# Optimization experiments

Measured on AMD Instinct MI355X. Metric: run time of the kernel, lower is better.

The kernel has to match this reference:

```python
import jax, jax.numpy as jnp
import numpy as np

TAU = 2.0          # LIF membrane time constant (spikingjelly default)
ALPHA = 2.0        # ATan surrogate width
EPS = 1e-5         # BatchNorm eps
NUM_HEADS = 8
SCALE = 0.125

@jax.custom_vjp
def spike(x):
    return (x >= 0.0).astype(x.dtype)

def _spike_fwd(x):
    return (x >= 0.0).astype(x.dtype), x

def _spike_bwd(x, g):
    # ATan surrogate gradient (spikingjelly default)
    return (g * (ALPHA / 2.0) / (1.0 + (jnp.pi / 2.0 * ALPHA * x) ** 2),)

spike.defvjp(_spike_fwd, _spike_bwd)

def lif(x, v_th):
    # Multi-step LIF over leading time axis T; hard reset to 0, v_reset=0.
    def step(v, xt):
        h = v + (xt - v) / TAU
        s = spike(h - v_th)
        return h * (1.0 - s), s
    _, s = jax.lax.scan(step, jnp.zeros_like(x[0]), x)
    return s

def bn(x, g, b, m, v):
    # BatchNorm1d in eval mode over channel (last) dim
    return (x - m) * jax.lax.rsqrt(v + EPS) * g + b

def setup_inputs() -> dict:
    key = jax.random.key(0)
    ks = jax.random.split(key, 16)
    T, B, N, C = 4, 16, 512, 512
    s = 1.0 / np.sqrt(C)
    inp = {"x": jax.random.normal(ks[0], (T, B, N, C), jnp.float32)}
    for i, p in enumerate("qkvp"):
        inp[f"w{p}"] = jax.random.normal(ks[1 + i], (C, C), jnp.float32) * s
        inp[f"b{p}"] = jnp.zeros((C,), jnp.float32)
        inp[f"{p}_gamma"] = jnp.ones((C,), jnp.float32)
        inp[f"{p}_beta"] = jnp.zeros((C,), jnp.float32)
        inp[f"{p}_mean"] = jax.random.normal(ks[5 + i], (C,), jnp.float32) * 0.1
        inp[f"{p}_var"] = jax.random.uniform(ks[9 + i], (C,), jnp.float32, minval=0.5, maxval=1.5)
    return inp

def reference(x, wq, bq, q_gamma, q_beta, q_mean, q_var,
              wk, bk, k_gamma, k_beta, k_mean, k_var,
              wv, bv, v_gamma, v_beta, v_mean, v_var,
              wp, bp, p_gamma, p_beta, p_mean, p_var):
    T, B, N, C = x.shape
    H = NUM_HEADS
    D = C // H

    def branch(w, b, g, be, m, va):
        y = bn(x @ w.T + b, g, be, m, va)          # Linear -> BN1d (eval)
        y = lif(y, 1.0)                             # spiking activation
        return y.reshape(T, B, N, H, D).transpose(0, 1, 3, 2, 4)  # [T,B,H,N,D]

    q = branch(wq, bq, q_gamma, q_beta, q_mean, q_var)
    k = branch(wk, bk, k_gamma, k_beta, k_mean, k_var)
    v = branch(wv, bv, v_gamma, v_beta, v_mean, v_var)

    attn = jnp.einsum('tbhnd,tbhmd->tbhnm', q, k) * SCALE  # [T,B,H,N,N]
    o = jnp.einsum('tbhnm,tbhmd->tbhnd', attn, v)          # [T,B,H,N,D]
    o = o.transpose(0, 1, 3, 2, 4).reshape(T, B, N, C)
    o = lif(o, 0.5)                                        # attn_lif, v_th=0.5
    o = bn(o @ wp.T + bp, p_gamma, p_beta, p_mean, p_var)
    return lif(o, 1.0)
```

## Files before the change

### kernel.cpp

```cpp
#include <hip/hip_runtime.h>
#include <hip/hip_bf16.h>
#include <hip/hip_fp16.h>
#include <cstddef>
#include <cstdint>

#define T_ 4
#define B_ 16
#define N_ 512
#define C_ 512
#define H_ 8
#define D_ 64
#define BN_T (B_*N_)

typedef unsigned short u16;
typedef __attribute__((ext_vector_type(8))) short bf16x8;
typedef __attribute__((ext_vector_type(8))) _Float16 f16x8;
typedef __attribute__((ext_vector_type(8))) unsigned short u16x8;
typedef __attribute__((ext_vector_type(4))) float f32x4;

__device__ __forceinline__ u16 f2bf_exact(float f) {
    union { float f; unsigned u; } x; x.f = f; return (u16)(x.u >> 16);
}
__device__ __forceinline__ void split2(float f, u16& h1, u16& h2) {
    const __half a = __float2half(f);
    const float r = (f - __half2float(a)) * 2048.0f;
    const __half b = __float2half(r);
    h1 = __half_as_ushort(a); h2 = __half_as_ushort(b);
}
__device__ __forceinline__ int swz(int rr, int q) {
    return (rr << 6) + (((q ^ ((rr >> 1) & 3)) & 3) << 4);
}
__device__ __forceinline__ int SW(int row, int col) {
    return (row << 6) + (col ^ ((row & 7) << 3));
}
__device__ __forceinline__ void gload16(const void* g, void* l) {
    __builtin_amdgcn_global_load_lds(
        (const __attribute__((address_space(1))) unsigned int*)g,
        (__attribute__((address_space(3))) unsigned int*)l, 16, 0, 0);
}

__global__ __launch_bounds__(256) void k_split_x(
    const float* __restrict__ x, u16* __restrict__ x1t, u16* __restrict__ x2t)
{
    const int tile = blockIdx.x;
    const int mt = tile >> 4, kb = tile & 15;
    const int tid = threadIdx.x;
    const int rr = tid >> 1, kh = tid & 1;
    const int t = rr & 3, bn = mt * 32 + (rr >> 2);
    const float* src = x + ((size_t)t * BN_T + bn) * C_ + kb * 32 + kh * 16;
    float f[16];
    *reinterpret_cast<float4*>(f + 0)  = *reinterpret_cast<const float4*>(src + 0);
    *reinterpret_cast<float4*>(f + 4)  = *reinterpret_cast<const float4*>(src + 4);
    *reinterpret_cast<float4*>(f + 8)  = *reinterpret_cast<const float4*>(src + 8);
    *reinterpret_cast<float4*>(f + 12) = *reinterpret_cast<const float4*>(src + 12);
    char* d1 = (char*)(x1t + ((size_t)tile << 12));
    char* d2 = (char*)(x2t + ((size_t)tile << 12));
    #pragma unroll
    for (int j = 0; j < 2; ++j) {
        u16x8 p1, p2;
        #pragma unroll
        for (int e = 0; e < 8; ++e) { u16 h1, h2; split2(f[8*j+e], h1, h2); p1[e] = h1; p2[e] = h2; }
        const int q = 2 * kh + j;
        *reinterpret_cast<u16x8*>(d1 + swz(rr, q)) = p1;
        *reinterpret_cast<u16x8*>(d2 + swz(rr, q)) = p2;
    }
}

__global__ __launch_bounds__(256) void k_split_w(
    const float* __restrict__ w, u16* __restrict__ w1t, u16* __restrict__ w2t)
{
    const int tile = blockIdx.x;
    const int nt = tile >> 4, kb = tile & 15;
    const int tid = threadIdx.x;
    const int rr = tid >> 1, kh = tid & 1;
    const int c = nt * 128 + rr;
    const float* src = w + (size_t)c * C_ + kb * 32 + kh * 16;
    float f[16];
    *reinterpret_cast<float4*>(f + 0)  = *reinterpret_cast<const float4*>(src + 0);
    *reinterpret_cast<float4*>(f + 4)  = *reinterpret_cast<const float4*>(src + 4);
    *reinterpret_cast<float4*>(f + 8)  = *reinterpret_cast<const float4*>(src + 8);
    *reinterpret_cast<float4*>(f + 12) = *reinterpret_cast<const float4*>(src + 12);
    char* d1 = (char*)(w1t + ((size_t)tile << 12));
    char* d2 = (char*)(w2t + ((size_t)tile << 12));
    #pragma unroll
    for (int j = 0; j < 2; ++j) {
        u16x8 p1, p2;
        #pragma unroll
        for (int e = 0; e < 8; ++e) { u16 h1, h2; split2(f[8*j+e], h1, h2); p1[e] = h1; p2[e] = h2; }
        const int q = 2 * kh + j;
        *reinterpret_cast<u16x8*>(d1 + swz(rr, q)) = p1;
        *reinterpret_cast<u16x8*>(d2 + swz(rr, q)) = p2;
    }
}

template<int MODE>
__global__ __launch_bounds__(256, 2) void k_linear_mfma(
    const u16* __restrict__ a1t, const u16* __restrict__ a2t,
    const u16* __restrict__ w1t, const u16* __restrict__ w2t,
    const float* __restrict__ bias, const float* __restrict__ gamma,
    const float* __restrict__ beta, const float* __restrict__ mean,
    const float* __restrict__ var, void* __restrict__ outp)
{
    __shared__ u16 lds[2][4][4096];

    const int dd  = blockIdx.x;
    const int lid = (dd & 7) * 128 + (dd >> 3);
    const int mt  = lid >> 2;
    const int nt  = lid & 3;
    const int bn0 = mt * 32;
    const int c0  = nt * 128;

    const int tid = threadIdx.x;
    const int wv  = tid >> 6, lane = tid & 63;
    const int l15 = tid & 15, g = (tid & 63) >> 4;
    const int go  = wv * 2048 + lane * 16;
    const int lo  = wv * 2048;

    f32x4 accA[2][8], accB[2][8];
    #pragma unroll
    for (int rt = 0; rt < 2; ++rt)
        #pragma unroll
        for (int ct = 0; ct < 8; ++ct) { accA[rt][ct] = {0,0,0,0}; accB[rt][ct] = {0,0,0,0}; }

    const size_t abase = (size_t)mt * 16, bbase = (size_t)nt * 16;

    auto stage = [&](int buf, int kb) {
        char* L = (char*)&lds[buf][0][0];
        const char* ga1 = (const char*)(a1t + ((abase + kb) << 12)) + go;
        const char* gb1 = (const char*)(w1t + ((bbase + kb) << 12)) + go;
        const char* gb2 = (const char*)(w2t + ((bbase + kb) << 12)) + go;
        gload16(ga1,        L + lo);
        gload16(ga1 + 1024, L + lo + 1024);
        if (MODE == 0) {
            const char* ga2 = (const char*)(a2t + ((abase + kb) << 12)) + go;
            gload16(ga2,        L + 8192 + lo);
            gload16(ga2 + 1024, L + 8192 + lo + 1024);
        }
        gload16(gb1,        L + 16384 + lo);
        gload16(gb1 + 1024, L + 16384 + lo + 1024);
        gload16(gb2,        L + 24576 + lo);
        gload16(gb2 + 1024, L + 24576 + lo + 1024);
    };

    stage(0, 0);
    __syncthreads();

    #pragma unroll 1
    for (int kb = 0; kb < 16; ++kb) {
        const int buf = kb & 1;
        if (kb < 15) stage(buf ^ 1, kb + 1);
        const char* L = (const char*)&lds[buf][0][0];
        f16x8 a1[2], a2[2];
        #pragma unroll
        for (int rt = 0; rt < 2; ++rt) {
            const int rr = wv * 32 + rt * 16 + l15;
            a1[rt] = *reinterpret_cast<const f16x8*>(L + swz(rr, g));
            if (MODE == 0)
                a2[rt] = *reinterpret_cast<const f16x8*>(L + 8192 + swz(rr, g));
        }
        #pragma unroll
        for (int ct = 0; ct < 8; ++ct) {
            const int rr2 = ct * 16 + l15;
            const f16x8 b1 = *reinterpret_cast<const f16x8*>(L + 16384 + swz(rr2, g));
            const f16x8 b2 = *reinterpret_cast<const f16x8*>(L + 24576 + swz(rr2, g));
            #pragma unroll
            for (int rt = 0; rt < 2; ++rt) {
                accA[rt][ct] = __builtin_amdgcn_mfma_f32_16x16x32_f16(a1[rt], b1, accA[rt][ct], 0, 0, 0);
                if (MODE == 0)
                    accB[rt][ct] = __builtin_amdgcn_mfma_f32_16x16x32_f16(a2[rt], b1, accB[rt][ct], 0, 0, 0);
                accB[rt][ct] = __builtin_amdgcn_mfma_f32_16x16x32_f16(a1[rt], b2, accB[rt][ct], 0, 0, 0);
            }
        }
        __syncthreads();
    }

    #pragma unroll
    for (int ct = 0; ct < 8; ++ct) {
        const int c = c0 + ct * 16 + l15;
        const float rs = 1.0f / sqrtf(var[c] + 1e-5f);
        const float ga = gamma[c], be = beta[c], mu = mean[c], bi = bias[c];
        #pragma unroll
        for (int rt = 0; rt < 2; ++rt) {
            const int bn = bn0 + wv * 8 + rt * 4 + g;
            float vm = 0.f;
            #pragma unroll
            for (int r = 0; r < 4; ++r) {
                const float y = accA[rt][ct][r] + accB[rt][ct][r] * (1.0f / 2048.0f) + bi;
                const float ybn = (y - mu) * rs * ga + be;
                const float h = vm + (ybn - vm) * 0.5f;
                const bool sp = (h >= 1.0f);
                vm = sp ? 0.f : h;
                if (MODE == 0) {
                    const int b = bn >> 9, n = bn & 511;
                    const int hh = c >> 6, d2 = c & 63;
                    ((u16*)outp)[((((size_t)r * B_ + b) * H_ + hh) * N_ + n) * D_ + d2] = sp ? 0x3F80 : 0;
                } else {
                    ((float*)outp)[((size_t)r * BN_T + bn) * C_ + c] = sp ? 1.0f : 0.0f;
                }
            }
        }
    }
}

__global__ __launch_bounds__(256) void k_attn_mfma(
    const u16* __restrict__ qg, const u16* __restrict__ kg,
    const u16* __restrict__ vg, u16* __restrict__ s2t)
{
    __shared__ u16 ks[4096];
    __shared__ u16 vts[4096];
    __shared__ u16 ssb[4096];

    const int id  = blockIdx.x;
    const int lid = (id & 7) * 128 + (id >> 3);
    const int bh  = lid >> 3;
    const int n0  = (lid & 7) * 64;
    const int b   = bh >> 3, hh = bh & 7;

    const int tid  = threadIdx.x;
    const int w    = tid >> 6, lane = tid & 63;
    const int l15  = lane & 15, g = lane >> 4;
    const int krow = tid >> 4, kcol = (tid & 15) * 4;
    const int vkv  = (tid & 15) * 4, vd = (tid >> 4) * 4;

    f32x4 vmem[4], oacc[4];
    #pragma unroll
    for (int d0 = 0; d0 < 4; ++d0) { vmem[d0] = {0,0,0,0}; oacc[d0] = {0,0,0,0}; }

    ushort4 kpre[4], vpre[4];
    bf16x8 qpre[2], qa[2];

    auto prefetch = [&](int it2) {
        const int t2 = it2 >> 3, m0 = (it2 & 7) * 64;
        const size_t base2 = ((size_t)t2 * (B_ * H_) + bh) * (size_t)(N_ * D_);
        #pragma unroll
        for (int i = 0; i < 4; ++i)
            kpre[i] = *reinterpret_cast<const ushort4*>(kg + base2 + (size_t)(m0 + krow + 16 * i) * D_ + kcol);
        #pragma unroll
        for (int i = 0; i < 4; ++i)
            vpre[i] = *reinterpret_cast<const ushort4*>(vg + base2 + (size_t)(m0 + vkv + i) * D_ + vd);
        if ((it2 & 7) == 0) {
            qpre[0] = *reinterpret_cast<const bf16x8*>(qg + base2 + (size_t)(n0 + 16 * w + l15) * D_ + 8 * g);
            qpre[1] = *reinterpret_cast<const bf16x8*>(qg + base2 + (size_t)(n0 + 16 * w + l15) * D_ + 32 + 8 * g);
        }
    };

    prefetch(0);

    #pragma unroll 1
    for (int it = 0; it < 32; ++it) {
        const int t = it >> 3, jt = it & 7;
        if (jt == 0) { qa[0] = qpre[0]; qa[1] = qpre[1]; }

        #pragma unroll
        for (int i = 0; i < 4; ++i) {
            const int row = krow + 16 * i;
            *reinterpret_cast<ushort4*>(&ks[SW(row, kcol)]) = kpre[i];
        }
        #pragma unroll
        for (int j = 0; j < 4; ++j) {
            ushort4 wv4;
            wv4.x = (&vpre[0].x)[j]; wv4.y = (&vpre[1].x)[j];
            wv4.z = (&vpre[2].x)[j]; wv4.w = (&vpre[3].x)[j];
            *reinterpret_cast<ushort4*>(&vts[SW(vd + j, vkv)]) = wv4;
        }
        __syncthreads();
        if (it < 31) prefetch(it + 1);

        #pragma unroll
        for (int kvt = 0; kvt < 4; ++kvt) {
            f32x4 acc = {0.f, 0.f, 0.f, 0.f};
            #pragma unroll
            for (int c = 0; c < 2; ++c) {
                const bf16x8 kb = *reinterpret_cast<const bf16x8*>(
                    &ks[SW(16 * kvt + l15, 32 * c + 8 * g)]);
                acc = __builtin_amdgcn_mfma_f32_16x16x32_bf16(qa[c], kb, acc, 0, 0, 0);
            }
            #pragma unroll
            for (int r = 0; r < 4; ++r)
                ssb[w * 1024 + SW(4 * g + r, 16 * kvt + l15)] = f2bf_exact(acc[r] * 0.125f);
        }
        #pragma unroll
        for (int c = 0; c < 2; ++c) {
            const bf16x8 sa = *reinterpret_cast<const bf16x8*>(
                &ssb[w * 1024 + SW(l15, 32 * c + 8 * g)]);
            #pragma unroll
            for (int d0 = 0; d0 < 4; ++d0) {
                const bf16x8 vb = *reinterpret_cast<const bf16x8*>(
                    &vts[SW(16 * d0 + l15, 32 * c + 8 * g)]);
                oacc[d0] = __builtin_amdgcn_mfma_f32_16x16x32_bf16(sa, vb, oacc[d0], 0, 0, 0);
            }
        }
        __syncthreads();

        if (jt == 7) {
            #pragma unroll
            for (int d0 = 0; d0 < 4; ++d0) {
                const int c = hh * 64 + d0 * 16 + l15;
                const int kb2 = c >> 5, kq = (c >> 3) & 3, e = c & 7;
                #pragma unroll
                for (int r = 0; r < 4; ++r) {
                    const float h = vmem[d0][r] + (oacc[d0][r] - vmem[d0][r]) * 0.5f;
                    const bool sp = (h >= 0.5f);
                    vmem[d0][r] = sp ? 0.f : h;
                    const int n = n0 + 16 * w + 4 * g + r;
                    const int bn = b * 512 + n;
                    const int mt2 = bn >> 5;
                    const int rr2 = (bn & 31) * 4 + t;
                    const size_t off = (((size_t)mt2 * 16 + kb2) << 13) + (rr2 << 6)
                                     + (((kq ^ ((rr2 >> 1) & 3)) & 3) << 4) + (e << 1);
                    *(u16*)((char*)s2t + off) = sp ? 0x3C00 : 0;
                }
                oacc[d0] = {0.f, 0.f, 0.f, 0.f};
            }
        }
    }
}

extern "C" void kernel_launch(void* const* d_in, const int* in_sizes, int n_in,
                              void* d_out, int out_size, void* d_ws, size_t ws_size,
                              hipStream_t stream)
{
    const float* x = (const float*)d_in[0];
    const float* W[4]  = {(const float*)d_in[1],  (const float*)d_in[7],  (const float*)d_in[13], (const float*)d_in[19]};
    const float* Bi[4] = {(const float*)d_in[2],  (const float*)d_in[8],  (const float*)d_in[14], (const float*)d_in[20]};
    const float* Ga[4] = {(const float*)d_in[3],  (const float*)d_in[9],  (const float*)d_in[15], (const float*)d_in[21]};
    const float* Be[4] = {(const float*)d_in[4],  (const float*)d_in[10], (const float*)d_in[16], (const float*)d_in[22]};
    const float* Mu[4] = {(const float*)d_in[5],  (const float*)d_in[11], (const float*)d_in[17], (const float*)d_in[23]};
    const float* Va[4] = {(const float*)d_in[6],  (const float*)d_in[12], (const float*)d_in[18], (const float*)d_in[24]};

    const size_t SPK = (size_t)T_ * B_ * N_ * C_;
    const size_t WSZ = (size_t)C_ * C_;
    u16* qb  = (u16*)d_ws;
    u16* kbf = qb + SPK;
    u16* vbf = kbf + SPK;
    u16* x1t = vbf + SPK;
    u16* x2t = x1t + SPK;
    u16* wt  = x2t + SPK;
    u16* s2t = x1t;

    dim3 blk(256);
    k_split_x<<<4096, blk, 0, stream>>>(x, x1t, x2t);
    for (int i = 0; i < 4; ++i)
        k_split_w<<<64, blk, 0, stream>>>(W[i], wt + (2*i) * WSZ, wt + (2*i+1) * WSZ);

    k_linear_mfma<0><<<1024, blk, 0, stream>>>(x1t, x2t, wt + 0*WSZ, wt + 1*WSZ, Bi[0], Ga[0], Be[0], Mu[0], Va[0], qb);
    k_linear_mfma<0><<<1024, blk, 0, stream>>>(x1t, x2t, wt + 2*WSZ, wt + 3*WSZ, Bi[1], Ga[1], Be[1], Mu[1], Va[1], kbf);
    k_linear_mfma<0><<<1024, blk, 0, stream>>>(x1t, x2t, wt + 4*WSZ, wt + 5*WSZ, Bi[2], Ga[2], Be[2], Mu[2], Va[2], vbf);
    k_attn_mfma<<<1024, blk, 0, stream>>>(qb, kbf, vbf, s2t);
    k_linear_mfma<1><<<1024, blk, 0, stream>>>(s2t, x2t, wt + 6*WSZ, wt + 7*WSZ, Bi[3], Ga[3], Be[3], Mu[3], Va[3], d_out);
}
```

Before: 322.3 us.

## Restructure attention kernel with 512-thread blocks and double-buffered software pipeline

The attention kernel now runs 512 threads per block, each block covering 128 query rows, and launches half as many blocks. Half the threads load K tiles and the other half load V tiles. K, V and score tiles are double-buffered so that the QK^T product for tile j+1 overlaps the PV product for tile j, with one barrier pair per step. The 0.125 scale moves from the bf16 scores to the final accumulator, which changes where bf16 rounding happens. The cost is more LDS per block and fewer blocks, which may lower occupancy.

Result: no change. 323.4 us (+0.3%).

```diff
diff --git a/kernel.cpp b/kernel.cpp
--- a/kernel.cpp
+++ b/kernel.cpp
@@ -202,115 +202,141 @@
     }
 }
 
-__global__ __launch_bounds__(256) void k_attn_mfma(
+__global__ __launch_bounds__(512, 4) void k_attn_mfma(
     const u16* __restrict__ qg, const u16* __restrict__ kg,
     const u16* __restrict__ vg, u16* __restrict__ s2t)
 {
-    __shared__ u16 ks[4096];
-    __shared__ u16 vts[4096];
-    __shared__ u16 ssb[4096];
+    __shared__ u16 ks[2][4096];
+    __shared__ u16 vts[2][4096];
+    __shared__ u16 ssb[8][2][1024];
 
     const int id  = blockIdx.x;
-    const int lid = (id & 7) * 128 + (id >> 3);
-    const int bh  = lid >> 3;
-    const int n0  = (lid & 7) * 64;
+    const int lid = (id & 7) * 64 + (id >> 3);
+    const int bh  = lid >> 2;
+    const int qt  = lid & 3;
     const int b   = bh >> 3, hh = bh & 7;
 
     const int tid  = threadIdx.x;
     const int w    = tid >> 6, lane = tid & 63;
     const int l15  = lane & 15, g = lane >> 4;
-    const int krow = tid >> 4, kcol = (tid & 15) * 4;
-    const int vkv  = (tid & 15) * 4, vd = (tid >> 4) * 4;
+
+    const bool isK = (tid < 256);
+    const int st   = isK ? tid : tid - 256;
+    const int krow = st >> 4, kcol = (st & 15) * 4;
+    const int vkv  = (st & 15) * 4, vd = (st >> 4) * 4;
+
+    ushort4 pre[4];
+    bf16x8 qa[2];
 
     f32x4 vmem[4], oacc[4];
     #pragma unroll
-    for (int d0 = 0; d0 < 4; ++d0) { vmem[d0] = {0,0,0,0}; oacc[d0] = {0,0,0,0}; }
-
-    ushort4 kpre[4], vpre[4];
-    bf16x8 qpre[2], qa[2];
-
-    auto prefetch = [&](int it2) {
-        const int t2 = it2 >> 3, m0 = (it2 & 7) * 64;
-        const size_t base2 = ((size_t)t2 * (B_ * H_) + bh) * (size_t)(N_ * D_);
-        #pragma unroll
-        for (int i = 0; i < 4; ++i)
-            kpre[i] = *reinterpret_cast<const ushort4*>(kg + base2 + (size_t)(m0 + krow + 16 * i) * D_ + kcol);
-        #pragma unroll
-        for (int i = 0; i < 4; ++i)
-            vpre[i] = *reinterpret_cast<const ushort4*>(vg + base2 + (size_t)(m0 + vkv + i) * D_ + vd);
-        if ((it2 & 7) == 0) {
-            qpre[0] = *reinterpret_cast<const bf16x8*>(qg + base2 + (size_t)(n0 + 16 * w + l15) * D_ + 8 * g);
-            qpre[1] = *reinterpret_cast<const bf16x8*>(qg + base2 + (size_t)(n0 + 16 * w + l15) * D_ + 32 + 8 * g);
-        }
-    };
-
-    prefetch(0);
+    for (int d0 = 0; d0 < 4; ++d0) vmem[d0] = {0,0,0,0};
 
     #pragma unroll 1
-    for (int it = 0; it < 32; ++it) {
-        const int t = it >> 3, jt = it & 7;
-        if (jt == 0) { qa[0] = qpre[0]; qa[1] = qpre[1]; }
-
-        #pragma unroll
-        for (int i = 0; i < 4; ++i) {
-            const int row = krow + 16 * i;
-            *reinterpret_cast<ushort4*>(&ks[SW(row, kcol)]) = kpre[i];
-        }
-        #pragma unroll
-        for (int j = 0; j < 4; ++j) {
-            ushort4 wv4;
-            wv4.x = (&vpre[0].x)[j]; wv4.y = (&vpre[1].x)[j];
-            wv4.z = (&vpre[2].x)[j]; wv4.w = (&vpre[3].x)[j];
-            *reinterpret_cast<ushort4*>(&vts[SW(vd + j, vkv)]) = wv4;
-        }
+    for (int t = 0; t < T_; ++t) {
+        const size_t base = ((size_t)t * (B_ * H_) + bh) * (size_t)(N_ * D_);
+
+        auto prefetch = [&](int j2) {
+            const int m0 = j2 * 64;
+            if (isK) {
+                #pragma unroll
+                for (int i = 0; i < 4; ++i)
+                    pre[i] = *reinterpret_cast<const ushort4*>(
+                        kg + base + (size_t)(m0 + krow + 16 * i) * D_ + kcol);
+            } else {
+                #pragma unroll
+                for (int i = 0; i < 4; ++i)
+                    pre[i] = *reinterpret_cast<const ushort4*>(
+                        vg + base + (size_t)(m0 + vkv + i) * D_ + vd);
+            }
+        };
+        auto ldswrite = [&](int buf) {
+            if (isK) {
+                #pragma unroll
+                for (int i = 0; i < 4; ++i)
+                    *reinterpret_cast<ushort4*>(&ks[buf][SW(krow + 16 * i, kcol)]) = pre[i];
+            } else {
+                #pragma unroll
+                for (int j = 0; j < 4; ++j) {
+                    ushort4 wv4;
+                    wv4.x = (&pre[0].x)[j]; wv4.y = (&pre[1].x)[j];
+                    wv4.z = (&pre[2].x)[j]; wv4.w = (&pre[3].x)[j];
+                    *reinterpret_cast<ushort4*>(&vts[buf][SW(vd + j, vkv)]) = wv4;
+                }
+            }
+        };
+        auto qk = [&](int kbuf, int sbuf) {
+            u16* sb = &ssb[w][sbuf][0];
+            #pragma unroll
+            for (int kvt = 0; kvt < 4; ++kvt) {
+                f32x4 acc = {0.f, 0.f, 0.f, 0.f};
+                #pragma unroll
+                for (int c = 0; c < 2; ++c) {
+                    const bf16x8 kb = *reinterpret_cast<const bf16x8*>(
+                        &ks[kbuf][SW(16 * kvt + l15, 32 * c + 8 * g)]);
+                    acc = __builtin_amdgcn_mfma_f32_16x16x32_bf16(qa[c], kb, acc, 0, 0, 0);
+                }
+                #pragma unroll
+                for (int r = 0; r < 4; ++r)
+                    sb[SW(4 * g + r, 16 * kvt + l15)] = f2bf_exact(acc[r]);
+            }
+        };
+        auto pv = [&](int vbuf, int sbuf) {
+            const u16* sb = &ssb[w][sbuf][0];
+            #pragma unroll
+            for (int c = 0; c < 2; ++c) {
+                const bf16x8 sa = *reinterpret_cast<const bf16x8*>(
+                    &sb[SW(l15, 32 * c + 8 * g)]);
+                #pragma unroll
+                for (int d0 = 0; d0 < 4; ++d0) {
+                    const bf16x8 vb = *reinterpret_cast<const bf16x8*>(
+                        &vts[vbuf][SW(16 * d0 + l15, 32 * c + 8 * g)]);
+                    oacc[d0] = __builtin_amdgcn_mfma_f32_16x16x32_bf16(sa, vb, oacc[d0], 0, 0, 0);
+                }
+            }
+        };
+
+        prefetch(0);
+        {
+            const size_t qrow = base + (size_t)(qt * 128 + 16 * w + l15) * D_;
+            qa[0] = *reinterpret_cast<const bf16x8*>(qg + qrow + 8 * g);
+            qa[1] = *reinterpret_cast<const bf16x8*>(qg + qrow + 32 + 8 * g);
+        }
+        #pragma unroll
+        for (int d0 = 0; d0 < 4; ++d0) oacc[d0] = {0.f, 0.f, 0.f, 0.f};
+        ldswrite(0);
         __syncthreads();
-        if (it < 31) prefetch(it + 1);
-
-        #pragma unroll
-        for (int kvt = 0; kvt < 4; ++kvt) {
-            f32x4 acc = {0.f, 0.f, 0.f, 0.f};
-            #pragma unroll
-            for (int c = 0; c < 2; ++c) {
-                const bf16x8 kb = *reinterpret_cast<const bf16x8*>(
-                    &ks[SW(16 * kvt + l15, 32 * c + 8 * g)]);
-                acc = __builtin_amdgcn_mfma_f32_16x16x32_bf16(qa[c], kb, acc, 0, 0, 0);
-            }
-            #pragma unroll
-            for (int r = 0; r < 4; ++r)
-                ssb[w * 1024 + SW(4 * g + r, 16 * kvt + l15)] = f2bf_exact(acc[r] * 0.125f);
-        }
-        #pragma unroll
-        for (int c = 0; c < 2; ++c) {
-            const bf16x8 sa = *reinterpret_cast<const bf16x8*>(
-                &ssb[w * 1024 + SW(l15, 32 * c + 8 * g)]);
-            #pragma unroll
-            for (int d0 = 0; d0 < 4; ++d0) {
-                const bf16x8 vb = *reinterpret_cast<const bf16x8*>(
-                    &vts[SW(16 * d0 + l15, 32 * c + 8 * g)]);
-                oacc[d0] = __builtin_amdgcn_mfma_f32_16x16x32_bf16(sa, vb, oacc[d0], 0, 0, 0);
-            }
-        }
-        __syncthreads();
-
-        if (jt == 7) {
-            #pragma unroll
-            for (int d0 = 0; d0 < 4; ++d0) {
-                const int c = hh * 64 + d0 * 16 + l15;
-                const int kb2 = c >> 5, kq = (c >> 3) & 3, e = c & 7;
-                #pragma unroll
-                for (int r = 0; r < 4; ++r) {
-                    const float h = vmem[d0][r] + (oacc[d0][r] - vmem[d0][r]) * 0.5f;
-                    const bool sp = (h >= 0.5f);
-                    vmem[d0][r] = sp ? 0.f : h;
-                    const int n = n0 + 16 * w + 4 * g + r;
-                    const int bn = b * 512 + n;
-                    const int mt2 = bn >> 5;
-                    const int rr2 = (bn & 31) * 4 + t;
-                    const size_t off = (((size_t)mt2 * 16 + kb2) << 13) + (rr2 << 6)
-                                     + (((kq ^ ((rr2 >> 1) & 3)) & 3) << 4) + (e << 1);
-                    *(u16*)((char*)s2t + off) = sp ? 0x3C00 : 0;
-                }
-                oacc[d0] = {0.f, 0.f, 0.f, 0.f};
+        prefetch(1);
+        qk(0, 0);
+
+        #pragma unroll 1
+        for (int j = 0; j < 7; ++j) {
+            ldswrite((j + 1) & 1);
+            __syncthreads();
+            if (j < 6) prefetch(j + 2);
+            qk((j + 1) & 1, (j + 1) & 1);
+            pv(j & 1, j & 1);
+            __syncthreads();
+        }
+        pv(1, 1);
+
+        #pragma unroll
+        for (int d0 = 0; d0 < 4; ++d0) {
+            const int c = hh * 64 + d0 * 16 + l15;
+            const int kb2 = c >> 5, kq = (c >> 3) & 3, e = c & 7;
+            #pragma unroll
+            for (int r = 0; r < 4; ++r) {
+                const float o = oacc[d0][r] * 0.125f;
+                const float h = vmem[d0][r] + (o - vmem[d0][r]) * 0.5f;
+                const bool sp = (h >= 0.5f);
+                vmem[d0][r] = sp ? 0.f : h;
+                const int n = qt * 128 + 16 * w + 4 * g + r;
+                const int bn = b * 512 + n;
+                const int mt2 = bn >> 5;
+                const int rr2 = (bn & 31) * 4 + t;
+                const size_t off = (((size_t)mt2 * 16 + kb2) << 13) + (rr2 << 6)
+                                 + (((kq ^ ((rr2 >> 1) & 3)) & 3) << 4) + (e << 1);
+                *(u16*)((char*)s2t + off) = sp ? 0x3C00 : 0;
             }
         }
     }
@@ -346,6 +372,6 @@
     k_linear_mfma<0><<<1024, blk, 0, stream>>>(x1t, x2t, wt + 0*WSZ, wt + 1*WSZ, Bi[0], Ga[0], Be[0], Mu[0], Va[0], qb);
     k_linear_mfma<0><<<1024, blk, 0, stream>>>(x1t, x2t, wt + 2*WSZ, wt + 3*WSZ, Bi[1], Ga[1], Be[1], Mu[1], Va[1], kbf);
     k_linear_mfma<0><<<1024, blk, 0, stream>>>(x1t, x2t, wt + 4*WSZ, wt + 5*WSZ, Bi[2], Ga[2], Be[2], Mu[2], Va[2], vbf);
-    k_attn_mfma<<<1024, blk, 0, stream>>>(qb, kbf, vbf, s2t);
+    k_attn_mfma<<<512, dim3(512), 0, stream>>>(qb, kbf, vbf, s2t);
     k_linear_mfma<1><<<1024, blk, 0, stream>>>(s2t, x2t, wt + 6*WSZ, wt + 7*WSZ, Bi[3], Ga[3], Be[3], Mu[3], Va[3], d_out);
 }
```
